# Kernel tuning notes

Measured on AMD Instinct MI355X. Metric: run time of the kernel, lower is better.

## Reference

```python
import jax, jax.numpy as jnp
import numpy as np

MESSAGE_PASSES = 3
HID = 100        # hidden_node_features == message_size
EDGE_F = 4       # n_edge_features
OUT = 100        # readout output dim


def setup_inputs() -> dict:
    key = jax.random.key(0)
    ks = jax.random.split(key, 8)
    B, N = 32, 128
    nodes = jax.random.normal(ks[0], (B, N, HID), dtype=jnp.float32)
    edges = jax.random.uniform(ks[1], (B, N, N, EDGE_F), dtype=jnp.float32)
    s = 1.0 / np.sqrt(HID)
    Wv = jax.random.normal(ks[2], (HID, HID), dtype=jnp.float32) * s
    Ww = jax.random.normal(ks[3], (HID, HID), dtype=jnp.float32) * s
    We = jax.random.normal(ks[4], (EDGE_F, HID), dtype=jnp.float32) * (1.0 / np.sqrt(EDGE_F))
    Wu = jax.random.normal(ks[5], (2 * HID, HID), dtype=jnp.float32) * (1.0 / np.sqrt(2 * HID))
    Wr = jax.random.normal(ks[6], (2 * HID, OUT), dtype=jnp.float32) * (1.0 / np.sqrt(2 * HID))
    return {"nodes": nodes, "edges": edges, "Wv": Wv, "Ww": Ww, "We": We, "Wu": Wu, "Wr": Wr}


def reference(nodes, edges, Wv, Ww, We, Wu, Wr):
    # adjacency[b,v,w] = sum_e edges[b,v,w,e]; nonzero entries define the edge set
    adjacency = edges.sum(axis=-1)                       # [B,N,N]
    edge_mask = adjacency != 0                           # [B,N,N]
    node_mask = adjacency.sum(axis=-1) != 0              # [B,N]

    # edge feature projection is constant across message passes
    e_proj = jnp.einsum('bvwe,eh->bvwh', edges, We)      # [B,N,N,H]

    hidden = nodes                                       # hidden_node_features == node feat dim
    for _ in range(MESSAGE_PASSES):
        # message_terms for every (b, v, w) edge: relu(h_v Wv + h_w Ww + e_vw We)
        pre = (hidden @ Wv)[:, :, None, :] + (hidden @ Ww)[:, None, :, :] + e_proj
        mterms = jnp.where(edge_mask[..., None], jax.nn.relu(pre), 0.0)
        # (same_batch * same_node) matmul == segment-sum over neighbors w
        messages = mterms.sum(axis=2)                    # [B,N,H]
        # update only nodes that appear in the edge set (degree > 0)
        upd = jnp.tanh(jnp.concatenate([hidden, messages], axis=-1) @ Wu)
        hidden = jnp.where(node_mask[..., None], upd, hidden)

    # readout: masked sum-pool of per-node graph terms
    graph_terms = jax.nn.relu(jnp.concatenate([hidden, nodes], axis=-1) @ Wr)  # [B,N,OUT]
    output = jnp.where(node_mask[..., None], graph_terms, 0.0).sum(axis=1)     # [B,OUT]
    return output
```

## Files before the change

kernel.cpp:

```cpp
#include <hip/hip_runtime.h>
#include <math.h>

#define B_   32
#define N_   128
#define H_   100
#define ROWS (B_ * N_)
#define RH   (ROWS * H_)
#define OUTSZ (B_ * H_)

__global__ __launch_bounds__(256, 6) void k_proj0(const float* __restrict__ nodes,
                                                  const float* __restrict__ Wv,
                                                  const float* __restrict__ Ww,
                                                  float* __restrict__ hv,
                                                  float* __restrict__ hw,
                                                  float* __restrict__ out) {
    __shared__ float nod_s[2][H_];
    const int row0 = blockIdx.x * 2;
    const int t = threadIdx.x, r = t >> 7, j = t & 127;
    {
        const int gid = blockIdx.x * 256 + t;
        if (gid < OUTSZ) out[gid] = 0.f;
    }
    {
        const float4* ng = (const float4*)(nodes + (size_t)row0 * H_);
        if (t < 50) ((float4*)nod_s)[t] = ng[t];
    }
    __syncthreads();
    if (j >= H_) return;
    const float4* h4p = (const float4*)nod_s[r];
    float va = 0.f, wa = 0.f;
#pragma unroll 5
    for (int k4 = 0; k4 < 25; ++k4) {
        const float4 h4 = h4p[k4];
        const int k = k4 * 4;
        va = fmaf(h4.x, Wv[(k + 0) * H_ + j], va);
        wa = fmaf(h4.x, Ww[(k + 0) * H_ + j], wa);
        va = fmaf(h4.y, Wv[(k + 1) * H_ + j], va);
        wa = fmaf(h4.y, Ww[(k + 1) * H_ + j], wa);
        va = fmaf(h4.z, Wv[(k + 2) * H_ + j], va);
        wa = fmaf(h4.z, Ww[(k + 2) * H_ + j], wa);
        va = fmaf(h4.w, Wv[(k + 3) * H_ + j], va);
        wa = fmaf(h4.w, Ww[(k + 3) * H_ + j], wa);
    }
    hv[(size_t)(row0 + r) * H_ + j] = va;
    hw[(size_t)(row0 + r) * H_ + j] = wa;
}

__global__ __launch_bounds__(256, 6) void k_pass(const float* __restrict__ edges,
                                                 const float* __restrict__ We,
                                                 const float* __restrict__ Wu,
                                                 const float* __restrict__ Wv,
                                                 const float* __restrict__ Ww,
                                                 const float* __restrict__ Wr,
                                                 const float* __restrict__ nodes,
                                                 float* __restrict__ hv_io,
                                                 const float* __restrict__ hw_in,
                                                 float* __restrict__ hw_out,
                                                 const float* __restrict__ hid_in,
                                                 float* __restrict__ hidden,
                                                 float* __restrict__ out,
                                                 int mode) {
    __shared__ float4 e_s[2][N_];
    __shared__ float  asum_part[4];
    __shared__ float  hid_s[2][H_];
    __shared__ float  msg_s[2][H_];
    __shared__ float  hn_s[2][H_];
    __shared__ float  nod_s[2][H_];
    __shared__ float  red_s[2][H_];

    const int row0 = blockIdx.x * 2;
    const int b = row0 >> 7;
    const int t = threadIdx.x, r = t >> 7, j = t & 127;
    const int wv = t >> 6, lane = t & 63;
    const int row = row0 + r;
    const bool act = (j < H_);

    {
        const float4* eg = (const float4*)(edges + (size_t)row0 * N_ * 4);
        const float4 e = eg[t];
        e_s[r][j] = e;
        float s = (e.x + e.y) + (e.z + e.w);
#pragma unroll
        for (int off = 32; off > 0; off >>= 1) s += __shfl_down(s, off);
        if (lane == 0) asum_part[wv] = s;
    }
    {
        const float4* hg = (const float4*)(hid_in + (size_t)row0 * H_);
        if (t < 50) ((float4*)hid_s)[t] = hg[t];
        if (mode == 2) {
            const float4* ng = (const float4*)(nodes + (size_t)row0 * H_);
            if (t < 50) ((float4*)nod_s)[t] = ng[t];
        }
    }
    __syncthreads();

    const float nm = ((asum_part[2 * r] + asum_part[2 * r + 1]) != 0.f) ? 1.f : 0.f;

    if (act) {
        const float hvv = hv_io[(size_t)row * H_ + j];
        const float we0 = We[0 * H_ + j], we1 = We[1 * H_ + j];
        const float we2 = We[2 * H_ + j], we3 = We[3 * H_ + j];
        const float* hwp = hw_in + (size_t)b * N_ * H_ + j;
        float acc = 0.f;
#pragma unroll 8
        for (int w = 0; w < N_; ++w) {
            const float4 e = e_s[r][w];
            const float  hww = hwp[w * H_];
            const float  s = (e.x + e.y) + (e.z + e.w);
            const float  m = (s != 0.f) ? 1.f : 0.f;
            float p = hvv + hww;
            p = fmaf(e.x, we0, p);
            p = fmaf(e.y, we1, p);
            p = fmaf(e.z, we2, p);
            p = fmaf(e.w, we3, p);
            acc = fmaf(m, fmaxf(p, 0.f), acc);
        }
        msg_s[r][j] = acc;
    }
    __syncthreads();

    if (act) {
        const float4* h4p = (const float4*)hid_s[r];
        const float4* m4p = (const float4*)msg_s[r];
        float u = 0.f;
#pragma unroll 5
        for (int k4 = 0; k4 < 25; ++k4) {
            const float4 h4 = h4p[k4];
            const int k = k4 * 4;
            u = fmaf(h4.x, Wu[(k + 0) * H_ + j], u);
            u = fmaf(h4.y, Wu[(k + 1) * H_ + j], u);
            u = fmaf(h4.z, Wu[(k + 2) * H_ + j], u);
            u = fmaf(h4.w, Wu[(k + 3) * H_ + j], u);
        }
#pragma unroll 5
        for (int k4 = 0; k4 < 25; ++k4) {
            const float4 m4 = m4p[k4];
            const int k = H_ + k4 * 4;
            u = fmaf(m4.x, Wu[(k + 0) * H_ + j], u);
            u = fmaf(m4.y, Wu[(k + 1) * H_ + j], u);
            u = fmaf(m4.z, Wu[(k + 2) * H_ + j], u);
            u = fmaf(m4.w, Wu[(k + 3) * H_ + j], u);
        }
        const float nh = (nm != 0.f) ? tanhf(u) : hid_s[r][j];
        hn_s[r][j] = nh;
        if (mode == 1) hidden[(size_t)row * H_ + j] = nh;
    }
    __syncthreads();

    if (mode == 1) {
        if (act) {
            const float4* h4p = (const float4*)hn_s[r];
            float va = 0.f, wa = 0.f;
#pragma unroll 5
            for (int k4 = 0; k4 < 25; ++k4) {
                const float4 h4 = h4p[k4];
                const int k = k4 * 4;
                va = fmaf(h4.x, Wv[(k + 0) * H_ + j], va);
                wa = fmaf(h4.x, Ww[(k + 0) * H_ + j], wa);
                va = fmaf(h4.y, Wv[(k + 1) * H_ + j], va);
                wa = fmaf(h4.y, Ww[(k + 1) * H_ + j], wa);
                va = fmaf(h4.z, Wv[(k + 2) * H_ + j], va);
                wa = fmaf(h4.z, Ww[(k + 2) * H_ + j], wa);
                va = fmaf(h4.w, Wv[(k + 3) * H_ + j], va);
                wa = fmaf(h4.w, Ww[(k + 3) * H_ + j], wa);
            }
            hv_io[(size_t)row * H_ + j] = va;
            hw_out[(size_t)row * H_ + j] = wa;
        }
    } else {
        if (act) {
            const float4* h4p = (const float4*)hn_s[r];
            const float4* n4p = (const float4*)nod_s[r];
            float u = 0.f;
#pragma unroll 5
            for (int k4 = 0; k4 < 25; ++k4) {
                const float4 h4 = h4p[k4];
                const int k = k4 * 4;
                u = fmaf(h4.x, Wr[(k + 0) * H_ + j], u);
                u = fmaf(h4.y, Wr[(k + 1) * H_ + j], u);
                u = fmaf(h4.z, Wr[(k + 2) * H_ + j], u);
                u = fmaf(h4.w, Wr[(k + 3) * H_ + j], u);
            }
#pragma unroll 5
            for (int k4 = 0; k4 < 25; ++k4) {
                const float4 n4 = n4p[k4];
                const int k = H_ + k4 * 4;
                u = fmaf(n4.x, Wr[(k + 0) * H_ + j], u);
                u = fmaf(n4.y, Wr[(k + 1) * H_ + j], u);
                u = fmaf(n4.z, Wr[(k + 2) * H_ + j], u);
                u = fmaf(n4.w, Wr[(k + 3) * H_ + j], u);
            }
            red_s[r][j] = nm * fmaxf(u, 0.f);
        }
        __syncthreads();
        if (t < H_) atomicAdd(out + b * H_ + t, red_s[0][t] + red_s[1][t]);
    }
}

extern "C" void kernel_launch(void* const* d_in, const int* in_sizes, int n_in,
                              void* d_out, int out_size, void* d_ws, size_t ws_size,
                              hipStream_t stream) {
    const float* nodes = (const float*)d_in[0];
    const float* edges = (const float*)d_in[1];
    const float* Wv    = (const float*)d_in[2];
    const float* Ww    = (const float*)d_in[3];
    const float* We    = (const float*)d_in[4];
    const float* Wu    = (const float*)d_in[5];
    const float* Wr    = (const float*)d_in[6];
    float* out = (float*)d_out;

    float* hidden = (float*)d_ws;
    float* hv     = hidden + RH;
    float* hwA    = hv + RH;
    float* hwB    = hwA + RH;

    k_proj0<<<ROWS / 2, 256, 0, stream>>>(nodes, Wv, Ww, hv, hwA, out);

    k_pass<<<ROWS / 2, 256, 0, stream>>>(edges, We, Wu, Wv, Ww, Wr, nodes,
                                         hv, hwA, hwB, nodes, hidden, out, 1);
    k_pass<<<ROWS / 2, 256, 0, stream>>>(edges, We, Wu, Wv, Ww, Wr, nodes,
                                         hv, hwB, hwA, hidden, hidden, out, 1);
    k_pass<<<ROWS / 2, 256, 0, stream>>>(edges, We, Wu, Wv, Ww, Wr, nodes,
                                         hv, hwA, hwB, hidden, hidden, out, 2);
}
```

Baseline: 207.9 us.

## Split message loop across four wavefronts using readlane edge broadcast and ballot mask

Restructures the per-edge message accumulation so each of the four wavefronts handles half of the neighbors for one row, with each lane computing two hidden channels via float2 loads. Edge features are broadcast from registers with readlane, and the edge mask comes from a wavefront ballot, so the shared-memory edge staging and the per-edge sum are no longer needed. Partial sums are combined through a small shared buffer at the cost of an extra barrier, and the occupancy hint is raised from 6 to 8. This removes idle lanes (threads with j≥100) and LDS traffic in the hot loop, but the full unroll of 64 readlanes may raise register pressure.

```diff
diff --git a/kernel.cpp b/kernel.cpp
--- a/kernel.cpp
+++ b/kernel.cpp
@@ -46,7 +46,7 @@
     hw[(size_t)(row0 + r) * H_ + j] = wa;
 }
 
-__global__ __launch_bounds__(256, 6) void k_pass(const float* __restrict__ edges,
+__global__ __launch_bounds__(256, 8) void k_pass(const float* __restrict__ edges,
                                                  const float* __restrict__ We,
                                                  const float* __restrict__ Wu,
                                                  const float* __restrict__ Wv,
@@ -60,8 +60,8 @@
                                                  float* __restrict__ hidden,
                                                  float* __restrict__ out,
                                                  int mode) {
-    __shared__ float4 e_s[2][N_];
     __shared__ float  asum_part[4];
+    __shared__ float  msgp_s[4][H_];
     __shared__ float  hid_s[2][H_];
     __shared__ float  msg_s[2][H_];
     __shared__ float  hn_s[2][H_];
@@ -71,18 +71,19 @@
     const int row0 = blockIdx.x * 2;
     const int b = row0 >> 7;
     const int t = threadIdx.x, r = t >> 7, j = t & 127;
-    const int wv = t >> 6, lane = t & 63;
+    const int wv = t >> 6, l = t & 63;
     const int row = row0 + r;
     const bool act = (j < H_);
 
-    {
-        const float4* eg = (const float4*)(edges + (size_t)row0 * N_ * 4);
-        const float4 e = eg[t];
-        e_s[r][j] = e;
-        float s = (e.x + e.y) + (e.z + e.w);
+    const float4* eg = (const float4*)(edges + (size_t)row0 * N_ * 4);
+    const float4 emy = eg[t];
+    unsigned long long bal;
+    {
+        float s = (emy.x + emy.y) + (emy.z + emy.w);
+        bal = __ballot(s != 0.f);
 #pragma unroll
         for (int off = 32; off > 0; off >>= 1) s += __shfl_down(s, off);
-        if (lane == 0) asum_part[wv] = s;
+        if (l == 0) asum_part[wv] = s;
     }
     {
         const float4* hg = (const float4*)(hid_in + (size_t)row0 * H_);
@@ -94,30 +95,45 @@
     }
     __syncthreads();
 
+    {
+        const int mrow = row0 + (wv >> 1);
+        const int w0 = (wv & 1) * 64;
+        const int ll = (l < 50) ? l : 49;
+        const float2 hv2 = *(const float2*)(hv_io + (size_t)mrow * H_ + 2 * ll);
+        const float2 we0 = *(const float2*)(We + 0 * H_ + 2 * ll);
+        const float2 we1 = *(const float2*)(We + 1 * H_ + 2 * ll);
+        const float2 we2 = *(const float2*)(We + 2 * H_ + 2 * ll);
+        const float2 we3 = *(const float2*)(We + 3 * H_ + 2 * ll);
+        const float* hwbase = hw_in + ((size_t)b * N_ + w0) * H_ + 2 * ll;
+        const int exi = __float_as_int(emy.x);
+        const int eyi = __float_as_int(emy.y);
+        const int ezi = __float_as_int(emy.z);
+        const int ewi = __float_as_int(emy.w);
+        float acc0 = 0.f, acc1 = 0.f;
+#pragma unroll
+        for (int w = 0; w < 64; ++w) {
+            const float ex = __int_as_float(__builtin_amdgcn_readlane(exi, w));
+            const float ey = __int_as_float(__builtin_amdgcn_readlane(eyi, w));
+            const float ez = __int_as_float(__builtin_amdgcn_readlane(ezi, w));
+            const float ew = __int_as_float(__builtin_amdgcn_readlane(ewi, w));
+            const float2 hw2 = *(const float2*)(hwbase + (size_t)w * H_);
+            const float m = ((bal >> w) & 1ull) ? 1.f : 0.f;
+            float p0 = hv2.x + hw2.x, p1 = hv2.y + hw2.y;
+            p0 = fmaf(ex, we0.x, p0); p1 = fmaf(ex, we0.y, p1);
+            p0 = fmaf(ey, we1.x, p0); p1 = fmaf(ey, we1.y, p1);
+            p0 = fmaf(ez, we2.x, p0); p1 = fmaf(ez, we2.y, p1);
+            p0 = fmaf(ew, we3.x, p0); p1 = fmaf(ew, we3.y, p1);
+            acc0 = fmaf(m, fmaxf(p0, 0.f), acc0);
+            acc1 = fmaf(m, fmaxf(p1, 0.f), acc1);
+        }
+        if (l < 50) *(float2*)(&msgp_s[wv][2 * l]) = make_float2(acc0, acc1);
+    }
+    __syncthreads();
+
+    if (act) msg_s[r][j] = msgp_s[2 * r][j] + msgp_s[2 * r + 1][j];
+    __syncthreads();
+
     const float nm = ((asum_part[2 * r] + asum_part[2 * r + 1]) != 0.f) ? 1.f : 0.f;
-
-    if (act) {
-        const float hvv = hv_io[(size_t)row * H_ + j];
-        const float we0 = We[0 * H_ + j], we1 = We[1 * H_ + j];
-        const float we2 = We[2 * H_ + j], we3 = We[3 * H_ + j];
-        const float* hwp = hw_in + (size_t)b * N_ * H_ + j;
-        float acc = 0.f;
-#pragma unroll 8
-        for (int w = 0; w < N_; ++w) {
-            const float4 e = e_s[r][w];
-            const float  hww = hwp[w * H_];
-            const float  s = (e.x + e.y) + (e.z + e.w);
-            const float  m = (s != 0.f) ? 1.f : 0.f;
-            float p = hvv + hww;
-            p = fmaf(e.x, we0, p);
-            p = fmaf(e.y, we1, p);
-            p = fmaf(e.z, we2, p);
-            p = fmaf(e.w, we3, p);
-            acc = fmaf(m, fmaxf(p, 0.f), acc);
-        }
-        msg_s[r][j] = acc;
-    }
-    __syncthreads();
 
     if (act) {
         const float4* h4p = (const float4*)hid_s[r];
```

Result: slower. 246.8 us (+18.7%).
